# Optimization experiments

Hardware: AMD Instinct MI355X
Metric: run time of the kernel (lower is better)

## Reference

```python
import jax, jax.numpy as jnp
import numpy as np

MIN_NORM = 1e-15
BALL_EPS = 4e-3  # HGCN float32 boundary eps


def _artanh(x):
    x = jnp.clip(x, -1.0 + 1e-7, 1.0 - 1e-7)
    return 0.5 * (jnp.log1p(x) - jnp.log1p(-x))


def _norm(x):
    return jnp.clip(jnp.linalg.norm(x, axis=-1, keepdims=True), MIN_NORM)


def proj(x, c):
    norm = _norm(x)
    maxnorm = (1.0 - BALL_EPS) / jnp.sqrt(c)
    return jnp.where(norm > maxnorm, x / norm * maxnorm, x)


def expmap0(u, c):
    sqrt_c = jnp.sqrt(c)
    u_norm = _norm(u)
    return jnp.tanh(sqrt_c * u_norm) * u / (sqrt_c * u_norm)


def logmap0(p, c):
    sqrt_c = jnp.sqrt(c)
    p_norm = _norm(p)
    return _artanh(sqrt_c * p_norm) * p / (sqrt_c * p_norm)


def mobius_add(x, y, c):
    x2 = jnp.sum(x * x, axis=-1, keepdims=True)
    y2 = jnp.sum(y * y, axis=-1, keepdims=True)
    xy = jnp.sum(x * y, axis=-1, keepdims=True)
    num = (1.0 + 2.0 * c * xy + c * y2) * x + (1.0 - c * x2) * y
    denom = 1.0 + 2.0 * c * xy + c * c * x2 * y2
    return num / jnp.clip(denom, MIN_NORM)


def mobius_matvec(m, x, c):
    sqrt_c = jnp.sqrt(c)
    x_norm = _norm(x)
    mx = x @ m.T  # [N, out]
    mx_norm = _norm(mx)
    res = jnp.tanh(mx_norm / x_norm * _artanh(sqrt_c * x_norm)) * mx / (mx_norm * sqrt_c)
    zero_row = jnp.all(mx == 0, axis=-1, keepdims=True)
    return jnp.where(zero_row, jnp.zeros_like(res), res)


def setup_inputs() -> dict:
    key = jax.random.key(0)
    k1, k2, k3, k4, k5 = jax.random.split(key, 5)
    N, D, C, E = 100000, 256, 128, 1600000
    x_tan = jax.random.normal(k1, (N, D), dtype=jnp.float32) * 1e-3  # small tangent vecs
    x = proj(expmap0(x_tan, 1.0), 1.0)  # valid points on Poincare ball
    edge_index = jax.random.randint(k2, (2, E), 0, N, dtype=jnp.int32)
    edge_weight = jax.random.uniform(k3, (E,), dtype=jnp.float32) / 16.0  # ~1/deg
    weight = jax.random.normal(k4, (C, D), dtype=jnp.float32) * (1.0 / np.sqrt(D))
    bias = jax.random.normal(k5, (C,), dtype=jnp.float32) * 0.01
    return {"x": x, "edge_index": edge_index, "edge_weight": edge_weight,
            "weight": weight, "bias": bias}


def reference(x, edge_index, edge_weight, weight, bias):
    c = 1.0
    N = x.shape[0]
    # HypLinear: mobius matvec + hyperbolic bias add (dropout=0)
    h = proj(mobius_matvec(weight, x, c), c)
    hyp_bias = proj(expmap0(bias[None, :], c), c)
    h = proj(mobius_add(h, hyp_bias, c), c)
    # HypAgg: logmap0 -> spmm(adj, x_tangent) -> expmap0
    x_t = logmap0(h, c)  # [N, C]
    row, col = edge_index[0], edge_index[1]
    msgs = x_t[col] * edge_weight[:, None]  # gather sources, weight
    agg = jax.ops.segment_sum(msgs, row, num_segments=N)  # scatter to dests
    h = proj(expmap0(agg, c), c)
    # HypAct with identity act, c_in == c_out
    h = proj(expmap0(logmap0(h, c), c), c)
    return h
```

## Files before the change

kernel.cpp:

```cpp
#include <hip/hip_runtime.h>
#include <math.h>

#define MAXNORM 0.996f
#define MIN_NORM 1e-15f

typedef __attribute__((ext_vector_type(8))) short short8;
typedef __attribute__((ext_vector_type(4))) float f32x4;

__device__ __forceinline__ float artanhf_(float x) {
    x = fminf(fmaxf(x, -1.0f + 1e-7f), 1.0f - 1e-7f);
    return 0.5f * (log1pf(x) - log1pf(-x));
}

__device__ __forceinline__ unsigned short f2bf(float f) {
    unsigned u = __float_as_uint(f);
    unsigned r = u + 0x7fffu + ((u >> 16) & 1u);
    return (unsigned short)(r >> 16);
}

__global__ void bias_kernel(const float* __restrict__ bias, float* __restrict__ bh) {
    const int l = threadIdx.x;
    float b0 = bias[2 * l], b1 = bias[2 * l + 1];
    float p = b0 * b0 + b1 * b1;
    for (int m = 1; m < 64; m <<= 1) p += __shfl_xor(p, m, 64);
    float n = fmaxf(sqrtf(p), MIN_NORM);
    float sc = tanhf(n) / n;
    float nn = tanhf(n);
    if (nn > MAXNORM) sc *= MAXNORM / nn;
    float h0 = sc * b0, h1 = sc * b1;
    bh[2 * l]     = h0;
    bh[2 * l + 1] = h1;
    float p2 = h0 * h0 + h1 * h1;
    for (int m = 1; m < 64; m <<= 1) p2 += __shfl_xor(p2, m, 64);
    if (l == 0) bh[128] = p2;
}

__global__ __launch_bounds__(256) void prep_x(
    const float* __restrict__ x, unsigned short* __restrict__ xb,
    float* __restrict__ xn, int N)
{
    const int wv = threadIdx.x >> 6, l = threadIdx.x & 63;
    for (int r = blockIdx.x * 4 + wv; r < N; r += gridDim.x * 4) {
        float4 v = ((const float4*)(x + (size_t)r * 256))[l];
        float p = v.x * v.x + v.y * v.y + v.z * v.z + v.w * v.w;
        for (int m = 1; m < 64; m <<= 1) p += __shfl_xor(p, m, 64);
        ushort4 o;
        o.x = f2bf(v.x); o.y = f2bf(v.y); o.z = f2bf(v.z); o.w = f2bf(v.w);
        ((ushort4*)(xb + (size_t)r * 256))[l] = o;
        if (l == 0) xn[r] = p;
    }
}

__global__ __launch_bounds__(256) void prep_w(
    const float* __restrict__ W, unsigned short* __restrict__ wb)
{
    int i = blockIdx.x * 256 + threadIdx.x;
    wb[i] = f2bf(W[i]);
}

__global__ __launch_bounds__(256) void linear_mfma(
    const unsigned short* __restrict__ xb, const unsigned short* __restrict__ wb,
    const float* __restrict__ xn, const float* __restrict__ bh,
    float* __restrict__ xt, int N)
{
    __shared__ float part[4][32][2];
    __shared__ float ab[32][2];
    __shared__ float y2s;

    const int t = threadIdx.x;
    const int w = t >> 6, l = t & 63;
    const int lo = l & 15, hi = l >> 4;
    const int row0 = blockIdx.x * 32;
    if (t == 0) y2s = bh[128];

    short8 bf[2][8];
    #pragma unroll
    for (int cg = 0; cg < 2; ++cg) {
        const unsigned short* bp = wb + (size_t)(w * 32 + cg * 16 + lo) * 256 + hi * 8;
        #pragma unroll
        for (int ks = 0; ks < 8; ++ks)
            bf[cg][ks] = *(const short8*)(bp + ks * 32);
    }

    int ra0 = row0 + lo;      if (ra0 >= N) ra0 = N - 1;
    int ra1 = row0 + 16 + lo; if (ra1 >= N) ra1 = N - 1;
    const unsigned short* ap0 = xb + (size_t)ra0 * 256 + hi * 8;
    const unsigned short* ap1 = xb + (size_t)ra1 * 256 + hi * 8;

    f32x4 acc[2][2] = {};
    #pragma unroll
    for (int ks = 0; ks < 8; ++ks) {
        short8 a0 = *(const short8*)(ap0 + ks * 32);
        short8 a1 = *(const short8*)(ap1 + ks * 32);
        acc[0][0] = __builtin_amdgcn_mfma_f32_16x16x32_bf16(a0, bf[0][ks], acc[0][0], 0, 0, 0);
        acc[0][1] = __builtin_amdgcn_mfma_f32_16x16x32_bf16(a0, bf[1][ks], acc[0][1], 0, 0, 0);
        acc[1][0] = __builtin_amdgcn_mfma_f32_16x16x32_bf16(a1, bf[0][ks], acc[1][0], 0, 0, 0);
        acc[1][1] = __builtin_amdgcn_mfma_f32_16x16x32_bf16(a1, bf[1][ks], acc[1][1], 0, 0, 0);
    }

    float bhv0 = bh[w * 32 + lo];
    float bhv1 = bh[w * 32 + 16 + lo];

    float spm[2][4], spb[2][4];
    #pragma unroll
    for (int rg = 0; rg < 2; ++rg)
    #pragma unroll
    for (int r = 0; r < 4; ++r) {
        float m0 = acc[rg][0][r], m1 = acc[rg][1][r];
        float pm = m0 * m0 + m1 * m1;
        float pb = m0 * bhv0 + m1 * bhv1;
        #pragma unroll
        for (int mk = 1; mk < 16; mk <<= 1) {
            pm += __shfl_xor(pm, mk, 64);
            pb += __shfl_xor(pb, mk, 64);
        }
        spm[rg][r] = pm; spb[rg][r] = pb;
    }
    if (lo == 0) {
        #pragma unroll
        for (int rg = 0; rg < 2; ++rg)
        #pragma unroll
        for (int r = 0; r < 4; ++r) {
            int row = rg * 16 + hi * 4 + r;
            part[w][row][0] = spm[rg][r];
            part[w][row][1] = spb[rg][r];
        }
    }
    __syncthreads();

    if (t < 32) {
        const int row = t;
        float pmm = part[0][row][0] + part[1][row][0] + part[2][row][0] + part[3][row][0];
        float pmb = part[0][row][1] + part[1][row][1] + part[2][row][1] + part[3][row][1];
        int grow = row0 + row; if (grow >= N) grow = N - 1;
        float pxx = xn[grow];
        float y2 = y2s;
        float x_norm  = fmaxf(sqrtf(pxx), MIN_NORM);
        float mx_norm = fmaxf(sqrtf(pmm), MIN_NORM);
        float rs = tanhf(mx_norm / x_norm * artanhf_(x_norm)) / mx_norm;
        float nres = rs * mx_norm;
        float sh = (nres > MAXNORM) ? rs * (MAXNORM / nres) : rs;
        float x2 = sh * sh * pmm;
        float xy = sh * pmb;
        float A_ = 1.f + 2.f * xy + y2;
        float B_ = 1.f - x2;
        float den = fmaxf(1.f + 2.f * xy + x2 * y2, MIN_NORM);
        float p22 = (A_ * A_ * sh * sh * pmm + 2.f * A_ * sh * B_ * pmb + B_ * B_ * y2)
                    / (den * den);
        float n2 = fmaxf(sqrtf(p22), MIN_NORM);
        float g = 1.f, n3 = n2;
        if (n2 > MAXNORM) { g = MAXNORM / n2; n3 = MAXNORM; }
        float a = artanhf_(n3);
        float s = g * (a / fmaxf(n3, MIN_NORM));
        ab[row][0] = s * A_ * sh / den;
        ab[row][1] = s * B_ / den;
    }
    __syncthreads();

    #pragma unroll
    for (int rg = 0; rg < 2; ++rg)
    #pragma unroll
    for (int r = 0; r < 4; ++r) {
        int row = rg * 16 + hi * 4 + r;
        int grow = row0 + row;
        if (grow < N) {
            float alpha = ab[row][0], beta = ab[row][1];
            float* dst = xt + (size_t)grow * 128 + w * 32 + lo;
            dst[0]  = alpha * acc[rg][0][r] + beta * bhv0;
            dst[16] = alpha * acc[rg][1][r] + beta * bhv1;
        }
    }
}

__global__ __launch_bounds__(256) void count_kernel(
    const int* __restrict__ row, int* __restrict__ cnt, int E)
{
    int e = blockIdx.x * 256 + threadIdx.x;
    if (e < E) atomicAdd(&cnt[row[e]], 1);
}

__global__ __launch_bounds__(256) void scan1_kernel(
    const int* __restrict__ cnt, int* __restrict__ rowptr,
    int* __restrict__ bsum, int N)
{
    __shared__ int s[256];
    const int t = threadIdx.x;
    const int base = blockIdx.x * 1024 + t * 4;
    int v0 = (base + 0 < N) ? cnt[base + 0] : 0;
    int v1 = (base + 1 < N) ? cnt[base + 1] : 0;
    int v2 = (base + 2 < N) ? cnt[base + 2] : 0;
    int v3 = (base + 3 < N) ? cnt[base + 3] : 0;
    int tot = v0 + v1 + v2 + v3;
    s[t] = tot;
    __syncthreads();
    for (int off = 1; off < 256; off <<= 1) {
        int o = (t >= off) ? s[t - off] : 0;
        __syncthreads();
        s[t] += o;
        __syncthreads();
    }
    int excl = s[t] - tot;
    if (base + 0 < N) rowptr[base + 0] = excl;
    if (base + 1 < N) rowptr[base + 1] = excl + v0;
    if (base + 2 < N) rowptr[base + 2] = excl + v0 + v1;
    if (base + 3 < N) rowptr[base + 3] = excl + v0 + v1 + v2;
    if (t == 255) bsum[blockIdx.x] = s[255];
}

__global__ __launch_bounds__(256) void scan2_kernel(int* __restrict__ bsum, int nb)
{
    __shared__ int s[256];
    const int t = threadIdx.x;
    int v = (t < nb) ? bsum[t] : 0;
    s[t] = v;
    __syncthreads();
    for (int off = 1; off < 256; off <<= 1) {
        int o = (t >= off) ? s[t - off] : 0;
        __syncthreads();
        s[t] += o;
        __syncthreads();
    }
    if (t < nb) bsum[t] = s[t] - v;
}

__global__ __launch_bounds__(256) void scan3_kernel(
    int* __restrict__ rowptr, int* __restrict__ cursor,
    const int* __restrict__ bsum, int N, int E)
{
    int i = blockIdx.x * 256 + threadIdx.x;
    if (i < N) {
        int v = rowptr[i] + bsum[i >> 10];
        rowptr[i] = v;
        cursor[i] = v;
    }
    if (i == 0) rowptr[N] = E;
}

__global__ __launch_bounds__(256) void fill_kernel(
    const int* __restrict__ row, const int* __restrict__ col,
    const float* __restrict__ ew, int* __restrict__ cursor,
    int* __restrict__ csr_col, float* __restrict__ csr_w, int E)
{
    int e = blockIdx.x * 256 + threadIdx.x;
    if (e >= E) return;
    int pos = atomicAdd(&cursor[row[e]], 1);
    csr_col[pos] = col[e];
    csr_w[pos]   = ew[e];
}

__global__ __launch_bounds__(256) void gather_kernel(
    const float* __restrict__ xt, const int* __restrict__ rowptr,
    const int* __restrict__ csr_col, const float* __restrict__ csr_w,
    float* __restrict__ out, int N)
{
    const int wv = threadIdx.x >> 6, l = threadIdx.x & 63;
    const int r = blockIdx.x * 4 + wv;
    if (r >= N) return;
    const int beg = rowptr[r], end = rowptr[r + 1];
    float a0 = 0.f, a1 = 0.f;
    for (int base = beg; base < end; base += 64) {
        int cn = end - base; if (cn > 64) cn = 64;
        int   cl = 0; float wl = 0.f;
        if (base + l < end) { cl = csr_col[base + l]; wl = csr_w[base + l]; }
        for (int jj = 0; jj < cn; ++jj) {
            int   c = __shfl(cl, jj, 64);
            float w = __shfl(wl, jj, 64);
            float2 v = ((const float2*)(xt + (size_t)c * 128))[l];
            a0 = fmaf(w, v.x, a0);
            a1 = fmaf(w, v.y, a1);
        }
    }
    float p = a0 * a0 + a1 * a1;
    for (int m = 1; m < 64; m <<= 1) p += __shfl_xor(p, m, 64);
    float un = fmaxf(sqrtf(p), MIN_NORM);
    float th = tanhf(un);
    float s1 = th / un;
    float n1 = th;
    if (n1 > MAXNORM) { s1 *= MAXNORM / n1; n1 = MAXNORM; }
    float a  = artanhf_(n1);
    float s2 = a / fmaxf(n1, MIN_NORM);
    float ua = fmaxf(a, MIN_NORM);
    float t3 = tanhf(ua);
    float s3 = t3 / ua;
    float s4 = (t3 > MAXNORM) ? MAXNORM / t3 : 1.f;
    float s = s1 * s2 * s3 * s4;
    float2 o; o.x = s * a0; o.y = s * a1;
    ((float2*)(out + (size_t)r * 128))[l] = o;
}

#define RT 32
__global__ __launch_bounds__(256) void linear_kernel(
    const float* __restrict__ x, const float* __restrict__ W,
    const float* __restrict__ bh, float* __restrict__ xt, int N)
{
    __shared__ float xs[RT][256];
    __shared__ float ms[RT][128];
    __shared__ float bhs[128];
    __shared__ float y2s;

    const int t = threadIdx.x;
    const int row0 = blockIdx.x * RT;

    if (t < 128) bhs[t] = bh[t];
    if (t == 0) y2s = bh[128];

    #pragma unroll
    for (int i = 0; i < 8; ++i) {
        int f  = i * 256 + t;
        int r  = f >> 6;
        int c4 = f & 63;
        int gr = row0 + r; if (gr >= N) gr = N - 1;
        ((float4*)xs[r])[c4] = ((const float4*)(x + (size_t)gr * 256))[c4];
    }
    __syncthreads();

    const int j  = t & 127;
    const int r0 = (t >> 7) * 16;
    float acc[16];
    #pragma unroll
    for (int r = 0; r < 16; ++r) acc[r] = 0.f;

    const float4* Wj = (const float4*)(W + (size_t)j * 256);
    for (int k4 = 0; k4 < 64; ++k4) {
        float4 w = Wj[k4];
        #pragma unroll
        for (int r = 0; r < 16; ++r) {
            float4 xv = ((const float4*)xs[r0 + r])[k4];
            acc[r] += xv.x * w.x + xv.y * w.y + xv.z * w.z + xv.w * w.w;
        }
    }
    #pragma unroll
    for (int r = 0; r < 16; ++r) ms[r0 + r][j] = acc[r];
    __syncthreads();

    const int wv = t >> 6, l = t & 63;
    const float y2 = y2s;
    for (int rr = 0; rr < 8; ++rr) {
        int r = wv * 8 + rr;
        int grow = row0 + r;
        float m0 = ms[r][2 * l], m1 = ms[r][2 * l + 1];
        float b0 = bhs[2 * l],   b1 = bhs[2 * l + 1];
        float4 xv = ((const float4*)xs[r])[l];
        float pxx = xv.x * xv.x + xv.y * xv.y + xv.z * xv.z + xv.w * xv.w;
        float pmm = m0 * m0 + m1 * m1;
        float pmb = m0 * b0 + m1 * b1;
        for (int m = 1; m < 64; m <<= 1) {
            pxx += __shfl_xor(pxx, m, 64);
            pmm += __shfl_xor(pmm, m, 64);
            pmb += __shfl_xor(pmb, m, 64);
        }
        float x_norm  = fmaxf(sqrtf(pxx), MIN_NORM);
        float mx_norm = fmaxf(sqrtf(pmm), MIN_NORM);
        float rs = tanhf(mx_norm / x_norm * artanhf_(x_norm)) / mx_norm;
        float nres = rs * mx_norm;
        float sh = (nres > MAXNORM) ? rs * (MAXNORM / nres) : rs;
        float x2 = sh * sh * pmm;
        float xy = sh * pmb;
        float A = 1.f + 2.f * xy + y2;
        float B = 1.f - x2;
        float den = fmaxf(1.f + 2.f * xy + x2 * y2, MIN_NORM);
        float h20 = (A * sh * m0 + B * b0) / den;
        float h21 = (A * sh * m1 + B * b1) / den;
        float p22 = h20 * h20 + h21 * h21;
        for (int m = 1; m < 64; m <<= 1) p22 += __shfl_xor(p22, m, 64);
        float n2 = fmaxf(sqrtf(p22), MIN_NORM);
        float g = 1.f, n3 = n2;
        if (n2 > MAXNORM) { g = MAXNORM / n2; n3 = MAXNORM; }
        float a = artanhf_(n3);
        float s = g * (a / fmaxf(n3, MIN_NORM));
        if (grow < N) {
            float2 o; o.x = s * h20; o.y = s * h21;
            ((float2*)(xt + (size_t)grow * 128))[l] = o;
        }
    }
}

__global__ __launch_bounds__(256) void scatter_kernel(
    const float* __restrict__ xt, const int* __restrict__ row,
    const int* __restrict__ col, const float* __restrict__ ew,
    float* __restrict__ agg, int E)
{
    long g = (long)blockIdx.x * blockDim.x + threadIdx.x;
    long e = g >> 5;
    int  l = (int)(g & 31);
    if (e >= E) return;
    int r = row[e], c = col[e];
    float wv = ew[e];
    float4 v = ((const float4*)(xt + (size_t)c * 128))[l];
    float* dst = agg + (size_t)r * 128 + l * 4;
    atomicAdd(dst + 0, v.x * wv);
    atomicAdd(dst + 1, v.y * wv);
    atomicAdd(dst + 2, v.z * wv);
    atomicAdd(dst + 3, v.w * wv);
}

__global__ __launch_bounds__(256) void final_kernel(float* __restrict__ io, int N) {
    const int wv = threadIdx.x >> 6, l = threadIdx.x & 63;
    const int r = blockIdx.x * 4 + wv;
    if (r >= N) return;
    float2 v = ((const float2*)(io + (size_t)r * 128))[l];
    float p = v.x * v.x + v.y * v.y;
    for (int m = 1; m < 64; m <<= 1) p += __shfl_xor(p, m, 64);
    float un = fmaxf(sqrtf(p), MIN_NORM);
    float th = tanhf(un);
    float s1 = th / un;
    float n1 = th;
    if (n1 > MAXNORM) { s1 *= MAXNORM / n1; n1 = MAXNORM; }
    float a  = artanhf_(n1);
    float s2 = a / fmaxf(n1, MIN_NORM);
    float ua = fmaxf(a, MIN_NORM);
    float t3 = tanhf(ua);
    float s3 = t3 / ua;
    float s4 = (t3 > MAXNORM) ? MAXNORM / t3 : 1.f;
    float s = s1 * s2 * s3 * s4;
    float2 o; o.x = s * v.x; o.y = s * v.y;
    ((float2*)(io + (size_t)r * 128))[l] = o;
}

extern "C" void kernel_launch(void* const* d_in, const int* in_sizes, int n_in,
                              void* d_out, int out_size, void* d_ws, size_t ws_size,
                              hipStream_t stream) {
    const float* x    = (const float*)d_in[0];
    const int*   ei   = (const int*)d_in[1];
    const float* ew   = (const float*)d_in[2];
    const float* W    = (const float*)d_in[3];
    const float* bias = (const float*)d_in[4];

    const int N = in_sizes[0] / 256;
    const int E = in_sizes[2];
    float* out = (float*)d_out;
    char*  ws  = (char*)d_ws;

    size_t off = 0;
    float* bh = (float*)(ws + off);            off += 256 * sizeof(float);
    float* xn = (float*)(ws + off);            off += (((size_t)N + 3) & ~3ull) * sizeof(float);
    unsigned short* xb = (unsigned short*)(ws + off); off += (size_t)N * 256 * sizeof(unsigned short);
    unsigned short* wb = (unsigned short*)(ws + off); off += 32768 * sizeof(unsigned short);
    float* xt = (float*)(ws + off);            off += (size_t)N * 128 * sizeof(float);
    int* rowptr = (int*)(ws + off);            off += ((size_t)N + 16) * sizeof(int);
    int* cursor = (int*)(ws + off);            off += (size_t)N * sizeof(int);
    int* bsum   = (int*)(ws + off);            off += 4096 * sizeof(int);
    int* csr_col = (int*)(ws + off);           off += (size_t)E * sizeof(int);
    float* csr_w = (float*)(ws + off);         off += (size_t)E * sizeof(float);
    const size_t need_new = off;

    size_t off2 = 0;
    float* bh2 = (float*)(ws + off2);          off2 += 256 * sizeof(float);
    float* xt2 = (float*)(ws + off2);          off2 += (size_t)N * 128 * sizeof(float);
    int* rowptr2 = (int*)(ws + off2);          off2 += ((size_t)N + 16) * sizeof(int);
    int* cursor2 = (int*)(ws + off2);          off2 += (size_t)N * sizeof(int);
    int* bsum2   = (int*)(ws + off2);          off2 += 4096 * sizeof(int);
    int* csr_col2 = (int*)(ws + off2);         off2 += (size_t)E * sizeof(int);
    float* csr_w2 = (float*)(ws + off2);       off2 += (size_t)E * sizeof(float);
    const size_t need_old = off2;

    const int nb = (N + 1023) / 1024;

    if (ws_size >= need_new) {
        bias_kernel<<<1, 64, 0, stream>>>(bias, bh);
        prep_w<<<128, 256, 0, stream>>>(W, wb);
        prep_x<<<2048, 256, 0, stream>>>(x, xb, xn, N);
        linear_mfma<<<(N + 31) / 32, 256, 0, stream>>>(xb, wb, xn, bh, xt, N);
        hipMemsetAsync(rowptr, 0, (size_t)N * sizeof(int), stream);
        count_kernel<<<(E + 255) / 256, 256, 0, stream>>>(ei, rowptr, E);
        scan1_kernel<<<nb, 256, 0, stream>>>(rowptr, rowptr, bsum, N);
        scan2_kernel<<<1, 256, 0, stream>>>(bsum, nb);
        scan3_kernel<<<(N + 255) / 256, 256, 0, stream>>>(rowptr, cursor, bsum, N, E);
        fill_kernel<<<(E + 255) / 256, 256, 0, stream>>>(
            ei, ei + E, ew, cursor, csr_col, csr_w, E);
        gather_kernel<<<(N + 3) / 4, 256, 0, stream>>>(
            xt, rowptr, csr_col, csr_w, out, N);
    } else if (ws_size >= need_old) {
        bias_kernel<<<1, 64, 0, stream>>>(bias, bh2);
        linear_kernel<<<(N + RT - 1) / RT, 256, 0, stream>>>(x, W, bh2, xt2, N);
        hipMemsetAsync(rowptr2, 0, (size_t)N * sizeof(int), stream);
        count_kernel<<<(E + 255) / 256, 256, 0, stream>>>(ei, rowptr2, E);
        scan1_kernel<<<nb, 256, 0, stream>>>(rowptr2, rowptr2, bsum2, N);
        scan2_kernel<<<1, 256, 0, stream>>>(bsum2, nb);
        scan3_kernel<<<(N + 255) / 256, 256, 0, stream>>>(rowptr2, cursor2, bsum2, N, E);
        fill_kernel<<<(E + 255) / 256, 256, 0, stream>>>(
            ei, ei + E, ew, cursor2, csr_col2, csr_w2, E);
        gather_kernel<<<(N + 3) / 4, 256, 0, stream>>>(
            xt2, rowptr2, csr_col2, csr_w2, out, N);
    } else {
        bias_kernel<<<1, 64, 0, stream>>>(bias, bh2);
        linear_kernel<<<(N + RT - 1) / RT, 256, 0, stream>>>(x, W, bh2, xt2, N);
        hipMemsetAsync(out, 0, (size_t)N * 128 * sizeof(float), stream);
        long threads = (long)E * 32;
        scatter_kernel<<<(unsigned)((threads + 255) / 256), 256, 0, stream>>>(
            xt2, ei, ei + E, ew, out, E);
        final_kernel<<<(N + 3) / 4, 256, 0, stream>>>(out, N);
    }
}
```

Baseline: 544.5 us.

## Fuse x conversion into MFMA linear, store tangent features as bf16, pack CSR

Removes the separate prep_x pass: the linear kernel now reads fp32 x directly, computes row norms in-register and converts to bf16 on the fly. Intermediate tangent features are written as packed bf16 pairs (output columns interleaved), halving the bytes the random-access gather reads per edge. CSR column and weight are packed into one int2 array and gather uses readlane instead of shfl. This trades precision of the aggregated features (bf16 instead of fp32) for lower memory traffic; the old mid-size workspace path is dropped.

After: 542.2 us. About the same (-0.4%).

```diff
diff --git a/kernel.cpp b/kernel.cpp
--- a/kernel.cpp
+++ b/kernel.cpp
@@ -35,22 +35,6 @@
     if (l == 0) bh[128] = p2;
 }
 
-__global__ __launch_bounds__(256) void prep_x(
-    const float* __restrict__ x, unsigned short* __restrict__ xb,
-    float* __restrict__ xn, int N)
-{
-    const int wv = threadIdx.x >> 6, l = threadIdx.x & 63;
-    for (int r = blockIdx.x * 4 + wv; r < N; r += gridDim.x * 4) {
-        float4 v = ((const float4*)(x + (size_t)r * 256))[l];
-        float p = v.x * v.x + v.y * v.y + v.z * v.z + v.w * v.w;
-        for (int m = 1; m < 64; m <<= 1) p += __shfl_xor(p, m, 64);
-        ushort4 o;
-        o.x = f2bf(v.x); o.y = f2bf(v.y); o.z = f2bf(v.z); o.w = f2bf(v.w);
-        ((ushort4*)(xb + (size_t)r * 256))[l] = o;
-        if (l == 0) xn[r] = p;
-    }
-}
-
 __global__ __launch_bounds__(256) void prep_w(
     const float* __restrict__ W, unsigned short* __restrict__ wb)
 {
@@ -59,12 +43,12 @@
 }
 
 __global__ __launch_bounds__(256) void linear_mfma(
-    const unsigned short* __restrict__ xb, const unsigned short* __restrict__ wb,
-    const float* __restrict__ xn, const float* __restrict__ bh,
-    float* __restrict__ xt, int N)
+    const float* __restrict__ x, const unsigned short* __restrict__ wb,
+    const float* __restrict__ bh, unsigned int* __restrict__ xtb, int N)
 {
     __shared__ float part[4][32][2];
     __shared__ float ab[32][2];
+    __shared__ float xsum[32];
     __shared__ float y2s;
 
     const int t = threadIdx.x;
@@ -76,7 +60,7 @@
     short8 bf[2][8];
     #pragma unroll
     for (int cg = 0; cg < 2; ++cg) {
-        const unsigned short* bp = wb + (size_t)(w * 32 + cg * 16 + lo) * 256 + hi * 8;
+        const unsigned short* bp = wb + (size_t)(w * 32 + 2 * lo + cg) * 256 + hi * 8;
         #pragma unroll
         for (int ks = 0; ks < 8; ++ks)
             bf[cg][ks] = *(const short8*)(bp + ks * 32);
@@ -84,22 +68,41 @@
 
     int ra0 = row0 + lo;      if (ra0 >= N) ra0 = N - 1;
     int ra1 = row0 + 16 + lo; if (ra1 >= N) ra1 = N - 1;
-    const unsigned short* ap0 = xb + (size_t)ra0 * 256 + hi * 8;
-    const unsigned short* ap1 = xb + (size_t)ra1 * 256 + hi * 8;
+    const float* ap0 = x + (size_t)ra0 * 256 + hi * 8;
+    const float* ap1 = x + (size_t)ra1 * 256 + hi * 8;
 
     f32x4 acc[2][2] = {};
+    float p0 = 0.f, p1 = 0.f;
     #pragma unroll
     for (int ks = 0; ks < 8; ++ks) {
-        short8 a0 = *(const short8*)(ap0 + ks * 32);
-        short8 a1 = *(const short8*)(ap1 + ks * 32);
+        float4 f00 = *(const float4*)(ap0 + ks * 32);
+        float4 f01 = *(const float4*)(ap0 + ks * 32 + 4);
+        float4 f10 = *(const float4*)(ap1 + ks * 32);
+        float4 f11 = *(const float4*)(ap1 + ks * 32 + 4);
+        p0 += f00.x*f00.x + f00.y*f00.y + f00.z*f00.z + f00.w*f00.w
+            + f01.x*f01.x + f01.y*f01.y + f01.z*f01.z + f01.w*f01.w;
+        p1 += f10.x*f10.x + f10.y*f10.y + f10.z*f10.z + f10.w*f10.w
+            + f11.x*f11.x + f11.y*f11.y + f11.z*f11.z + f11.w*f11.w;
+        short8 a0, a1;
+        a0[0]=(short)f2bf(f00.x); a0[1]=(short)f2bf(f00.y);
+        a0[2]=(short)f2bf(f00.z); a0[3]=(short)f2bf(f00.w);
+        a0[4]=(short)f2bf(f01.x); a0[5]=(short)f2bf(f01.y);
+        a0[6]=(short)f2bf(f01.z); a0[7]=(short)f2bf(f01.w);
+        a1[0]=(short)f2bf(f10.x); a1[1]=(short)f2bf(f10.y);
+        a1[2]=(short)f2bf(f10.z); a1[3]=(short)f2bf(f10.w);
+        a1[4]=(short)f2bf(f11.x); a1[5]=(short)f2bf(f11.y);
+        a1[6]=(short)f2bf(f11.z); a1[7]=(short)f2bf(f11.w);
         acc[0][0] = __builtin_amdgcn_mfma_f32_16x16x32_bf16(a0, bf[0][ks], acc[0][0], 0, 0, 0);
         acc[0][1] = __builtin_amdgcn_mfma_f32_16x16x32_bf16(a0, bf[1][ks], acc[0][1], 0, 0, 0);
         acc[1][0] = __builtin_amdgcn_mfma_f32_16x16x32_bf16(a1, bf[0][ks], acc[1][0], 0, 0, 0);
         acc[1][1] = __builtin_amdgcn_mfma_f32_16x16x32_bf16(a1, bf[1][ks], acc[1][1], 0, 0, 0);
     }
-
-    float bhv0 = bh[w * 32 + lo];
-    float bhv1 = bh[w * 32 + 16 + lo];
+    p0 += __shfl_xor(p0, 16, 64); p0 += __shfl_xor(p0, 32, 64);
+    p1 += __shfl_xor(p1, 16, 64); p1 += __shfl_xor(p1, 32, 64);
+    if (w == 0 && hi == 0) { xsum[lo] = p0; xsum[16 + lo] = p1; }
+
+    float bhv0 = bh[w * 32 + 2 * lo];
+    float bhv1 = bh[w * 32 + 2 * lo + 1];
 
     float spm[2][4], spb[2][4];
     #pragma unroll
@@ -132,8 +135,7 @@
         const int row = t;
         float pmm = part[0][row][0] + part[1][row][0] + part[2][row][0] + part[3][row][0];
         float pmb = part[0][row][1] + part[1][row][1] + part[2][row][1] + part[3][row][1];
-        int grow = row0 + row; if (grow >= N) grow = N - 1;
-        float pxx = xn[grow];
+        float pxx = xsum[row];
         float y2 = y2s;
         float x_norm  = fmaxf(sqrtf(pxx), MIN_NORM);
         float mx_norm = fmaxf(sqrtf(pmm), MIN_NORM);
@@ -165,9 +167,10 @@
         int grow = row0 + row;
         if (grow < N) {
             float alpha = ab[row][0], beta = ab[row][1];
-            float* dst = xt + (size_t)grow * 128 + w * 32 + lo;
-            dst[0]  = alpha * acc[rg][0][r] + beta * bhv0;
-            dst[16] = alpha * acc[rg][1][r] + beta * bhv1;
+            float v0 = alpha * acc[rg][0][r] + beta * bhv0;
+            float v1 = alpha * acc[rg][1][r] + beta * bhv1;
+            unsigned int pk = (unsigned int)f2bf(v0) | ((unsigned int)f2bf(v1) << 16);
+            xtb[(size_t)grow * 64 + w * 16 + lo] = pk;
         }
     }
 }
@@ -239,19 +242,17 @@
 __global__ __launch_bounds__(256) void fill_kernel(
     const int* __restrict__ row, const int* __restrict__ col,
     const float* __restrict__ ew, int* __restrict__ cursor,
-    int* __restrict__ csr_col, float* __restrict__ csr_w, int E)
+    int2* __restrict__ csr, int E)
 {
     int e = blockIdx.x * 256 + threadIdx.x;
     if (e >= E) return;
     int pos = atomicAdd(&cursor[row[e]], 1);
-    csr_col[pos] = col[e];
-    csr_w[pos]   = ew[e];
-}
-
-__global__ __launch_bounds__(256) void gather_kernel(
-    const float* __restrict__ xt, const int* __restrict__ rowptr,
-    const int* __restrict__ csr_col, const float* __restrict__ csr_w,
-    float* __restrict__ out, int N)
+    csr[pos] = make_int2(col[e], __float_as_int(ew[e]));
+}
+
+__global__ __launch_bounds__(256) void gather_bf16(
+    const unsigned int* __restrict__ xtb, const int* __restrict__ rowptr,
+    const int2* __restrict__ csr, float* __restrict__ out, int N)
 {
     const int wv = threadIdx.x >> 6, l = threadIdx.x & 63;
     const int r = blockIdx.x * 4 + wv;
@@ -260,14 +261,16 @@
     float a0 = 0.f, a1 = 0.f;
     for (int base = beg; base < end; base += 64) {
         int cn = end - base; if (cn > 64) cn = 64;
-        int   cl = 0; float wl = 0.f;
-        if (base + l < end) { cl = csr_col[base + l]; wl = csr_w[base + l]; }
+        int cl = 0, wl = 0;
+        if (base + l < end) { int2 p = csr[base + l]; cl = p.x; wl = p.y; }
         for (int jj = 0; jj < cn; ++jj) {
-            int   c = __shfl(cl, jj, 64);
-            float w = __shfl(wl, jj, 64);
-            float2 v = ((const float2*)(xt + (size_t)c * 128))[l];
-            a0 = fmaf(w, v.x, a0);
-            a1 = fmaf(w, v.y, a1);
+            int   c = __builtin_amdgcn_readlane(cl, jj);
+            float w = __int_as_float(__builtin_amdgcn_readlane(wl, jj));
+            unsigned int u = xtb[(size_t)c * 64 + l];
+            float ce = __uint_as_float(u << 16);
+            float co = __uint_as_float(u & 0xffff0000u);
+            a0 = fmaf(w, ce, a0);
+            a1 = fmaf(w, co, a1);
         }
     }
     float p = a0 * a0 + a1 * a1;
@@ -432,26 +435,18 @@
     char*  ws  = (char*)d_ws;
 
     size_t off = 0;
-    float* bh = (float*)(ws + off);            off += 256 * sizeof(float);
-    float* xn = (float*)(ws + off);            off += (((size_t)N + 3) & ~3ull) * sizeof(float);
-    unsigned short* xb = (unsigned short*)(ws + off); off += (size_t)N * 256 * sizeof(unsigned short);
+    float* bh = (float*)(ws + off);                   off += 256 * sizeof(float);
     unsigned short* wb = (unsigned short*)(ws + off); off += 32768 * sizeof(unsigned short);
-    float* xt = (float*)(ws + off);            off += (size_t)N * 128 * sizeof(float);
-    int* rowptr = (int*)(ws + off);            off += ((size_t)N + 16) * sizeof(int);
-    int* cursor = (int*)(ws + off);            off += (size_t)N * sizeof(int);
-    int* bsum   = (int*)(ws + off);            off += 4096 * sizeof(int);
-    int* csr_col = (int*)(ws + off);           off += (size_t)E * sizeof(int);
-    float* csr_w = (float*)(ws + off);         off += (size_t)E * sizeof(float);
+    unsigned int* xtb = (unsigned int*)(ws + off);    off += (size_t)N * 64 * sizeof(unsigned int);
+    int* rowptr = (int*)(ws + off);                   off += ((size_t)N + 16) * sizeof(int);
+    int* cursor = (int*)(ws + off);                   off += (size_t)N * sizeof(int);
+    int* bsum   = (int*)(ws + off);                   off += 4096 * sizeof(int);
+    int2* csr   = (int2*)(ws + off);                  off += (size_t)E * sizeof(int2);
     const size_t need_new = off;
 
     size_t off2 = 0;
     float* bh2 = (float*)(ws + off2);          off2 += 256 * sizeof(float);
     float* xt2 = (float*)(ws + off2);          off2 += (size_t)N * 128 * sizeof(float);
-    int* rowptr2 = (int*)(ws + off2);          off2 += ((size_t)N + 16) * sizeof(int);
-    int* cursor2 = (int*)(ws + off2);          off2 += (size_t)N * sizeof(int);
-    int* bsum2   = (int*)(ws + off2);          off2 += 4096 * sizeof(int);
-    int* csr_col2 = (int*)(ws + off2);         off2 += (size_t)E * sizeof(int);
-    float* csr_w2 = (float*)(ws + off2);       off2 += (size_t)E * sizeof(float);
     const size_t need_old = off2;
 
     const int nb = (N + 1023) / 1024;
@@ -459,29 +454,16 @@
     if (ws_size >= need_new) {
         bias_kernel<<<1, 64, 0, stream>>>(bias, bh);
         prep_w<<<128, 256, 0, stream>>>(W, wb);
-        prep_x<<<2048, 256, 0, stream>>>(x, xb, xn, N);
-        linear_mfma<<<(N + 31) / 32, 256, 0, stream>>>(xb, wb, xn, bh, xt, N);
+        linear_mfma<<<(N + 31) / 32, 256, 0, stream>>>(x, wb, bh, xtb, N);
         hipMemsetAsync(rowptr, 0, (size_t)N * sizeof(int), stream);
         count_kernel<<<(E + 255) / 256, 256, 0, stream>>>(ei, rowptr, E);
         scan1_kernel<<<nb, 256, 0, stream>>>(rowptr, rowptr, bsum, N);
         scan2_kernel<<<1, 256, 0, stream>>>(bsum, nb);
         scan3_kernel<<<(N + 255) / 256, 256, 0, stream>>>(rowptr, cursor, bsum, N, E);
         fill_kernel<<<(E + 255) / 256, 256, 0, stream>>>(
-            ei, ei + E, ew, cursor, csr_col, csr_w, E);
-        gather_kernel<<<(N + 3) / 4, 256, 0, stream>>>(
-            xt, rowptr, csr_col, csr_w, out, N);
-    } else if (ws_size >= need_old) {
-        bias_kernel<<<1, 64, 0, stream>>>(bias, bh2);
-        linear_kernel<<<(N + RT - 1) / RT, 256, 0, stream>>>(x, W, bh2, xt2, N);
-        hipMemsetAsync(rowptr2, 0, (size_t)N * sizeof(int), stream);
-        count_kernel<<<(E + 255) / 256, 256, 0, stream>>>(ei, rowptr2, E);
-        scan1_kernel<<<nb, 256, 0, stream>>>(rowptr2, rowptr2, bsum2, N);
-        scan2_kernel<<<1, 256, 0, stream>>>(bsum2, nb);
-        scan3_kernel<<<(N + 255) / 256, 256, 0, stream>>>(rowptr2, cursor2, bsum2, N, E);
-        fill_kernel<<<(E + 255) / 256, 256, 0, stream>>>(
-            ei, ei + E, ew, cursor2, csr_col2, csr_w2, E);
-        gather_kernel<<<(N + 3) / 4, 256, 0, stream>>>(
-            xt2, rowptr2, csr_col2, csr_w2, out, N);
+            ei, ei + E, ew, cursor, csr, E);
+        gather_bf16<<<(N + 3) / 4, 256, 0, stream>>>(
+            xtb, rowptr, csr, out, N);
     } else {
         bias_kernel<<<1, 64, 0, stream>>>(bias, bh2);
         linear_kernel<<<(N + RT - 1) / RT, 256, 0, stream>>>(x, W, bh2, xt2, N);
```
